# Performance work log

Hardware: AMD Instinct MI355X
Metric: run time of the kernel (lower is better)

The kernel has to match this reference:

```python
import jax, jax.numpy as jnp
import numpy as np

BATCH, IN, OUT, G = 2048, 512, 512, 8


def setup_inputs() -> dict:
    key = jax.random.key(0)
    k1, k2, k3 = jax.random.split(key, 3)
    x = jax.random.normal(k1, (BATCH, IN), dtype=jnp.float32)
    # spline coefficients, initialized small like normal_(c, 0, 0.001)
    c = jax.random.normal(k2, (G, OUT, IN), dtype=jnp.float32) * 0.001
    # residual weights, xavier-like small init
    w_b = jax.random.normal(k3, (OUT, IN), dtype=jnp.float32) * 0.001
    w_s = jnp.ones((OUT, IN), dtype=jnp.float32)
    # RBF grid centers over [-2, 2] (get_size() == G)
    grid = jnp.arange(G, dtype=jnp.float32) * (4.0 / (G - 1)) - 2.0
    return {"x": x, "c": c, "w_b": w_b, "w_s": w_s, "grid": grid}


def _basis(x, grid):
    # Gaussian RBF basis: [batch, G, in]
    d = x[:, None, :] - grid[None, :, None]
    return jnp.exp(-(d * d))


def reference(x, c, w_b, w_s, grid):
    basis_vals = _basis(x, grid)                      # [b, n=G, i]
    # faithful to th.einsum('bni,aoi->boi', ...): n and a are independently summed
    spline_out = jnp.einsum('bni,aoi->boi', basis_vals, c)  # [b, o, i]
    spline_out = spline_out * w_s[None]
    res_out = jax.nn.silu(x)[:, None, :] * w_b[None]  # [b, o, i]
    return (spline_out + res_out).sum(axis=-1)        # [b, o]
```

## Files before the change

### kernel.cpp

```cpp
#include <hip/hip_runtime.h>

#define BATCH 2048
#define IN    512
#define OUT   512
#define NG    8
#define KTOT  1024

#define BM 64
#define BN 64
#define BK 64
#define PAD 88
#define NIT (KTOT / BK)

typedef __attribute__((ext_vector_type(8))) short bf16x8;
typedef __attribute__((ext_vector_type(4))) float f32x4;

__device__ inline unsigned short f2bf(float f) {
    union { float f; unsigned int u; } v; v.f = f;
    unsigned int r = v.u + 0x7fffu + ((v.u >> 16) & 1u);
    return (unsigned short)(r >> 16);
}

__global__ __launch_bounds__(256) void prep_kernel(const float* __restrict__ x,
                                                   const float* __restrict__ c,
                                                   const float* __restrict__ w_b,
                                                   const float* __restrict__ w_s,
                                                   const float* __restrict__ grid,
                                                   unsigned short* __restrict__ A,
                                                   unsigned short* __restrict__ B) {
    int blk = blockIdx.x;
    int tid = threadIdx.x;
    if (blk < 512) {
        int e = (blk * 256 + tid) * 8;
        float g0 = grid[0];
        float dl = grid[1] - g0;
        float d2 = dl * dl;
        float dn[NG];
#pragma unroll
        for (int n = 0; n < NG; ++n) dn[n] = __expf(-d2 * (float)(n * n));
        float4 x0 = *(const float4*)&x[e];
        float4 x1 = *(const float4*)&x[e + 4];
        float xv[8] = {x0.x, x0.y, x0.z, x0.w, x1.x, x1.y, x1.z, x1.w};
        unsigned short sv[8], lv[8];
#pragma unroll
        for (int j = 0; j < 8; ++j) {
            float u  = xv[j] - g0;
            float e1 = __expf(-u * u);
            float q  = __expf(2.f * dl * u);
            float p  = dn[NG - 1];
#pragma unroll
            for (int n = NG - 2; n >= 0; --n) p = p * q + dn[n];
            sv[j] = f2bf(e1 * p);
            lv[j] = f2bf(xv[j] / (1.f + __expf(-xv[j])));
        }
        int b = e >> 9, i = e & 511;
        *(int4*)&A[b * KTOT + i]       = *(int4*)sv;
        *(int4*)&A[b * KTOT + 512 + i] = *(int4*)lv;
    } else {
        int e = ((blk - 512) * 256 + tid) * 8;
        float acc[8] = {};
#pragma unroll
        for (int a = 0; a < NG; ++a) {
            float4 c0 = *(const float4*)&c[(size_t)a * (OUT * IN) + e];
            float4 c1 = *(const float4*)&c[(size_t)a * (OUT * IN) + e + 4];
            acc[0] += c0.x; acc[1] += c0.y; acc[2] += c0.z; acc[3] += c0.w;
            acc[4] += c1.x; acc[5] += c1.y; acc[6] += c1.z; acc[7] += c1.w;
        }
        float4 s0 = *(const float4*)&w_s[e];
        float4 s1 = *(const float4*)&w_s[e + 4];
        float sw[8] = {s0.x, s0.y, s0.z, s0.w, s1.x, s1.y, s1.z, s1.w};
        float4 b0 = *(const float4*)&w_b[e];
        float4 b1 = *(const float4*)&w_b[e + 4];
        float bw[8] = {b0.x, b0.y, b0.z, b0.w, b1.x, b1.y, b1.z, b1.w};
        unsigned short cv[8], bv[8];
#pragma unroll
        for (int j = 0; j < 8; ++j) { cv[j] = f2bf(acc[j] * sw[j]); bv[j] = f2bf(bw[j]); }
        int o = e >> 9, i = e & 511;
        *(int4*)&B[o * KTOT + i]       = *(int4*)cv;
        *(int4*)&B[o * KTOT + 512 + i] = *(int4*)bv;
    }
}

__global__ __launch_bounds__(512) void gemm_kernel(const unsigned short* __restrict__ A,
                                                   const unsigned short* __restrict__ B,
                                                   float* __restrict__ outp) {
    __shared__ short As[2][BM * PAD];
    __shared__ short Bs[2][BN * PAD];

    int tid  = threadIdx.x;
    int lane = tid & 63;
    int w    = tid >> 6;
    int wm   = w >> 1, wn = w & 1;
    int lr   = lane & 15, lg = lane >> 4;

    int bid  = blockIdx.x;
    int mg   = bid & 7;
    int rest = bid >> 3;
    int sub  = rest >> 3;
    int ncol = rest & 7;
    int m0   = (mg * 4 + sub) * BM;
    int n0   = ncol * BN;

    int srow = tid >> 3;
    int sc8  = tid & 7;

    const int4* Ag = (const int4*)&A[(size_t)(m0 + srow) * KTOT + sc8 * 8];
    const int4* Bg = (const int4*)&B[(size_t)(n0 + srow) * KTOT + sc8 * 8];

    int wo = srow * PAD + sc8 * 8;

    f32x4 acc0 = {0.f, 0.f, 0.f, 0.f};
    f32x4 acc1 = {0.f, 0.f, 0.f, 0.f};

    int4 ca = Ag[0], cb = Bg[0];
    *(int4*)&As[0][wo] = ca;
    *(int4*)&Bs[0][wo] = cb;
    ca = Ag[8]; cb = Bg[8];
    __syncthreads();

#pragma unroll
    for (int it = 0; it < NIT; ++it) {
        int cur = it & 1;
        if (it + 1 < NIT) {
            *(int4*)&As[cur ^ 1][wo] = ca;
            *(int4*)&Bs[cur ^ 1][wo] = cb;
            if (it + 2 < NIT) { ca = Ag[(it + 2) * 8]; cb = Bg[(it + 2) * 8]; }
        }
#pragma unroll
        for (int ks = 0; ks < 2; ++ks) {
            bf16x8 a  = *(const bf16x8*)&As[cur][(wm * 16 + lr)      * PAD + ks * 32 + lg * 8];
            bf16x8 b0 = *(const bf16x8*)&Bs[cur][(wn * 32 + lr)      * PAD + ks * 32 + lg * 8];
            bf16x8 b1 = *(const bf16x8*)&Bs[cur][(wn * 32 + 16 + lr) * PAD + ks * 32 + lg * 8];
            acc0 = __builtin_amdgcn_mfma_f32_16x16x32_bf16(a, b0, acc0, 0, 0, 0);
            acc1 = __builtin_amdgcn_mfma_f32_16x16x32_bf16(a, b1, acc1, 0, 0, 0);
        }
        __syncthreads();
    }

    int orow = m0 + wm * 16 + lg * 4;
    int ocol = n0 + wn * 32 + lr;
#pragma unroll
    for (int r = 0; r < 4; ++r) {
        outp[(size_t)(orow + r) * OUT + ocol]      = acc0[r];
        outp[(size_t)(orow + r) * OUT + ocol + 16] = acc1[r];
    }
}

extern "C" void kernel_launch(void* const* d_in, const int* in_sizes, int n_in,
                              void* d_out, int out_size, void* d_ws, size_t ws_size,
                              hipStream_t stream) {
    (void)in_sizes; (void)n_in; (void)out_size; (void)ws_size;
    const float* x    = (const float*)d_in[0];
    const float* c    = (const float*)d_in[1];
    const float* w_b  = (const float*)d_in[2];
    const float* w_s  = (const float*)d_in[3];
    const float* grid = (const float*)d_in[4];
    float* outp = (float*)d_out;

    unsigned short* A = (unsigned short*)d_ws;
    unsigned short* B = A + (size_t)BATCH * KTOT;

    prep_kernel<<<512 + 128, 256, 0, stream>>>(x, c, w_b, w_s, grid, A, B);
    gemm_kernel<<<(BATCH / BM) * (OUT / BN), 512, 0, stream>>>(A, B, outp);
}
```

Measured before the change: 17.73 us.

## Fuse prep and GEMM into one kernel with a grid-wide atomic barrier

Merges the prep kernel and the GEMM kernel into a single launch of 256 blocks. Each block first builds its share of the bf16 A and B operands, then all blocks wait on an agent-scope atomic counter before starting the MFMA GEMM. This removes the second kernel launch and the gap between kernels, at the cost of a memset launch, a spin-wait barrier, and the assumption that all 256 blocks are resident at the same time.

```diff
diff --git a/kernel.cpp b/kernel.cpp
--- a/kernel.cpp
+++ b/kernel.cpp
@@ -11,6 +11,7 @@
 #define BK 64
 #define PAD 88
 #define NIT (KTOT / BK)
+#define NBLK 256
 
 typedef __attribute__((ext_vector_type(8))) short bf16x8;
 typedef __attribute__((ext_vector_type(4))) float f32x4;
@@ -21,23 +22,37 @@
     return (unsigned short)(r >> 16);
 }
 
-__global__ __launch_bounds__(256) void prep_kernel(const float* __restrict__ x,
-                                                   const float* __restrict__ c,
-                                                   const float* __restrict__ w_b,
-                                                   const float* __restrict__ w_s,
-                                                   const float* __restrict__ grid,
-                                                   unsigned short* __restrict__ A,
-                                                   unsigned short* __restrict__ B) {
-    int blk = blockIdx.x;
-    int tid = threadIdx.x;
-    if (blk < 512) {
-        int e = (blk * 256 + tid) * 8;
+__global__ __launch_bounds__(512) void fused_kernel(const float* __restrict__ x,
+                                                    const float* __restrict__ c,
+                                                    const float* __restrict__ w_b,
+                                                    const float* __restrict__ w_s,
+                                                    const float* __restrict__ grid,
+                                                    unsigned short* __restrict__ A,
+                                                    unsigned short* __restrict__ B,
+                                                    float* __restrict__ outp,
+                                                    unsigned int* __restrict__ flag) {
+    __shared__ short As[2][BM * PAD];
+    __shared__ short Bs[2][BN * PAD];
+
+    int tid  = threadIdx.x;
+    int bid  = blockIdx.x;
+    int mg   = bid & 7;
+    int rest = bid >> 3;
+    int sub  = rest >> 3;
+    int ncol = rest & 7;
+    int m0   = (mg * 4 + sub) * BM;
+    int n0   = ncol * BN;
+
+    {
+        int row = m0 + ncol * 8 + (tid >> 6);
+        int col = (tid & 63) * 8;
         float g0 = grid[0];
         float dl = grid[1] - g0;
         float d2 = dl * dl;
         float dn[NG];
 #pragma unroll
         for (int n = 0; n < NG; ++n) dn[n] = __expf(-d2 * (float)(n * n));
+        int e = row * IN + col;
         float4 x0 = *(const float4*)&x[e];
         float4 x1 = *(const float4*)&x[e + 4];
         float xv[8] = {x0.x, x0.y, x0.z, x0.w, x1.x, x1.y, x1.z, x1.w};
@@ -53,11 +68,14 @@
             sv[j] = f2bf(e1 * p);
             lv[j] = f2bf(xv[j] / (1.f + __expf(-xv[j])));
         }
-        int b = e >> 9, i = e & 511;
-        *(int4*)&A[b * KTOT + i]       = *(int4*)sv;
-        *(int4*)&A[b * KTOT + 512 + i] = *(int4*)lv;
-    } else {
-        int e = ((blk - 512) * 256 + tid) * 8;
+        *(int4*)&A[row * KTOT + col]       = *(int4*)sv;
+        *(int4*)&A[row * KTOT + 512 + col] = *(int4*)lv;
+    }
+
+    if (tid < 128) {
+        int row = bid * 2 + (tid >> 6);
+        int col = (tid & 63) * 8;
+        int e = row * IN + col;
         float acc[8] = {};
 #pragma unroll
         for (int a = 0; a < NG; ++a) {
@@ -75,38 +93,28 @@
         unsigned short cv[8], bv[8];
 #pragma unroll
         for (int j = 0; j < 8; ++j) { cv[j] = f2bf(acc[j] * sw[j]); bv[j] = f2bf(bw[j]); }
-        int o = e >> 9, i = e & 511;
-        *(int4*)&B[o * KTOT + i]       = *(int4*)cv;
-        *(int4*)&B[o * KTOT + 512 + i] = *(int4*)bv;
+        *(int4*)&B[row * KTOT + col]       = *(int4*)cv;
+        *(int4*)&B[row * KTOT + 512 + col] = *(int4*)bv;
     }
-}
 
-__global__ __launch_bounds__(512) void gemm_kernel(const unsigned short* __restrict__ A,
-                                                   const unsigned short* __restrict__ B,
-                                                   float* __restrict__ outp) {
-    __shared__ short As[2][BM * PAD];
-    __shared__ short Bs[2][BN * PAD];
+    __syncthreads();
+    if (tid == 0)
+        __hip_atomic_fetch_add(flag, 1u, __ATOMIC_ACQ_REL, __HIP_MEMORY_SCOPE_AGENT);
+    while (__hip_atomic_load(flag, __ATOMIC_RELAXED, __HIP_MEMORY_SCOPE_AGENT) < NBLK)
+        __builtin_amdgcn_s_sleep(8);
+    (void)__hip_atomic_load(flag, __ATOMIC_ACQUIRE, __HIP_MEMORY_SCOPE_AGENT);
+    __syncthreads();
 
-    int tid  = threadIdx.x;
     int lane = tid & 63;
     int w    = tid >> 6;
     int wm   = w >> 1, wn = w & 1;
     int lr   = lane & 15, lg = lane >> 4;
-
-    int bid  = blockIdx.x;
-    int mg   = bid & 7;
-    int rest = bid >> 3;
-    int sub  = rest >> 3;
-    int ncol = rest & 7;
-    int m0   = (mg * 4 + sub) * BM;
-    int n0   = ncol * BN;
 
     int srow = tid >> 3;
     int sc8  = tid & 7;
 
     const int4* Ag = (const int4*)&A[(size_t)(m0 + srow) * KTOT + sc8 * 8];
     const int4* Bg = (const int4*)&B[(size_t)(n0 + srow) * KTOT + sc8 * 8];
-
     int wo = srow * PAD + sc8 * 8;
 
     f32x4 acc0 = {0.f, 0.f, 0.f, 0.f};
@@ -159,7 +167,8 @@
 
     unsigned short* A = (unsigned short*)d_ws;
     unsigned short* B = A + (size_t)BATCH * KTOT;
+    unsigned int* flag = (unsigned int*)((char*)d_ws + (8u << 20));
 
-    prep_kernel<<<512 + 128, 256, 0, stream>>>(x, c, w_b, w_s, grid, A, B);
-    gemm_kernel<<<(BATCH / BM) * (OUT / BN), 512, 0, stream>>>(A, B, outp);
+    hipMemsetAsync(flag, 0, sizeof(unsigned int), stream);
+    fused_kernel<<<NBLK, 512, 0, stream>>>(x, c, w_b, w_s, grid, A, B, outp, flag);
 }
```

Result: slower. 63.82 us (+259.9%).

## Split GEMM K across two blocks and within-block warps, reduce with atomics

Applied to the files above, without the earlier changes.

The GEMM kernel now splits the K dimension in half across two blocks, which doubles the grid to 512 blocks and halves the serial k-loop length. Inside each block the warps are re-partitioned so that warp pairs split the two k-substeps, and each warp computes a 32x32 tile with four MFMAs. Partial sums from the two k-substeps are reduced through shared memory. The two block halves are combined with float atomic adds into an output that is zeroed first with a memset. This targets the short serial loop and low occupancy of the original 256-block launch, at the cost of an extra memset, atomic traffic and a non-deterministic summation order.

```diff
diff --git a/kernel.cpp b/kernel.cpp
--- a/kernel.cpp
+++ b/kernel.cpp
@@ -10,7 +10,7 @@
 #define BN 64
 #define BK 64
 #define PAD 88
-#define NIT (KTOT / BK)
+#define NITH 8
 
 typedef __attribute__((ext_vector_type(8))) short bf16x8;
 typedef __attribute__((ext_vector_type(4))) float f32x4;
@@ -90,12 +90,16 @@
     int tid  = threadIdx.x;
     int lane = tid & 63;
     int w    = tid >> 6;
-    int wm   = w >> 1, wn = w & 1;
+    int wm   = (w >> 2) & 1;
+    int wn   = (w >> 1) & 1;
+    int ks   = w & 1;
     int lr   = lane & 15, lg = lane >> 4;
 
-    int bid  = blockIdx.x;
-    int mg   = bid & 7;
-    int rest = bid >> 3;
+    int bid   = blockIdx.x;
+    int tile  = bid & 255;
+    int khalf = bid >> 8;
+    int mg   = tile & 7;
+    int rest = tile >> 3;
     int sub  = rest >> 3;
     int ncol = rest & 7;
     int m0   = (mg * 4 + sub) * BM;
@@ -104,13 +108,14 @@
     int srow = tid >> 3;
     int sc8  = tid & 7;
 
-    const int4* Ag = (const int4*)&A[(size_t)(m0 + srow) * KTOT + sc8 * 8];
-    const int4* Bg = (const int4*)&B[(size_t)(n0 + srow) * KTOT + sc8 * 8];
-
+    const int4* Ag = (const int4*)&A[(size_t)(m0 + srow) * KTOT + khalf * (NITH * BK) + sc8 * 8];
+    const int4* Bg = (const int4*)&B[(size_t)(n0 + srow) * KTOT + khalf * (NITH * BK) + sc8 * 8];
     int wo = srow * PAD + sc8 * 8;
 
-    f32x4 acc0 = {0.f, 0.f, 0.f, 0.f};
-    f32x4 acc1 = {0.f, 0.f, 0.f, 0.f};
+    f32x4 acc00 = {0.f, 0.f, 0.f, 0.f};
+    f32x4 acc01 = {0.f, 0.f, 0.f, 0.f};
+    f32x4 acc10 = {0.f, 0.f, 0.f, 0.f};
+    f32x4 acc11 = {0.f, 0.f, 0.f, 0.f};
 
     int4 ca = Ag[0], cb = Bg[0];
     *(int4*)&As[0][wo] = ca;
@@ -119,30 +124,47 @@
     __syncthreads();
 
 #pragma unroll
-    for (int it = 0; it < NIT; ++it) {
+    for (int it = 0; it < NITH; ++it) {
         int cur = it & 1;
-        if (it + 1 < NIT) {
+        if (it + 1 < NITH) {
             *(int4*)&As[cur ^ 1][wo] = ca;
             *(int4*)&Bs[cur ^ 1][wo] = cb;
-            if (it + 2 < NIT) { ca = Ag[(it + 2) * 8]; cb = Bg[(it + 2) * 8]; }
+            if (it + 2 < NITH) { ca = Ag[(it + 2) * 8]; cb = Bg[(it + 2) * 8]; }
         }
-#pragma unroll
-        for (int ks = 0; ks < 2; ++ks) {
-            bf16x8 a  = *(const bf16x8*)&As[cur][(wm * 16 + lr)      * PAD + ks * 32 + lg * 8];
-            bf16x8 b0 = *(const bf16x8*)&Bs[cur][(wn * 32 + lr)      * PAD + ks * 32 + lg * 8];
-            bf16x8 b1 = *(const bf16x8*)&Bs[cur][(wn * 32 + 16 + lr) * PAD + ks * 32 + lg * 8];
-            acc0 = __builtin_amdgcn_mfma_f32_16x16x32_bf16(a, b0, acc0, 0, 0, 0);
-            acc1 = __builtin_amdgcn_mfma_f32_16x16x32_bf16(a, b1, acc1, 0, 0, 0);
-        }
+        bf16x8 a0 = *(const bf16x8*)&As[cur][(wm * 32 + lr)      * PAD + ks * 32 + lg * 8];
+        bf16x8 a1 = *(const bf16x8*)&As[cur][(wm * 32 + 16 + lr) * PAD + ks * 32 + lg * 8];
+        bf16x8 b0 = *(const bf16x8*)&Bs[cur][(wn * 32 + lr)      * PAD + ks * 32 + lg * 8];
+        bf16x8 b1 = *(const bf16x8*)&Bs[cur][(wn * 32 + 16 + lr) * PAD + ks * 32 + lg * 8];
+        acc00 = __builtin_amdgcn_mfma_f32_16x16x32_bf16(a0, b0, acc00, 0, 0, 0);
+        acc01 = __builtin_amdgcn_mfma_f32_16x16x32_bf16(a0, b1, acc01, 0, 0, 0);
+        acc10 = __builtin_amdgcn_mfma_f32_16x16x32_bf16(a1, b0, acc10, 0, 0, 0);
+        acc11 = __builtin_amdgcn_mfma_f32_16x16x32_bf16(a1, b1, acc11, 0, 0, 0);
         __syncthreads();
     }
 
-    int orow = m0 + wm * 16 + lg * 4;
-    int ocol = n0 + wn * 32 + lr;
+    float* Ls = (float*)&As[0][0];
+    int p = w >> 1;
+    if (ks == 1) {
+        *(f32x4*)&Ls[p * 1024 + lane * 16 + 0]  = acc00;
+        *(f32x4*)&Ls[p * 1024 + lane * 16 + 4]  = acc01;
+        *(f32x4*)&Ls[p * 1024 + lane * 16 + 8]  = acc10;
+        *(f32x4*)&Ls[p * 1024 + lane * 16 + 12] = acc11;
+    }
+    __syncthreads();
+    if (ks == 0) {
+        f32x4 p00 = *(const f32x4*)&Ls[p * 1024 + lane * 16 + 0];
+        f32x4 p01 = *(const f32x4*)&Ls[p * 1024 + lane * 16 + 4];
+        f32x4 p10 = *(const f32x4*)&Ls[p * 1024 + lane * 16 + 8];
+        f32x4 p11 = *(const f32x4*)&Ls[p * 1024 + lane * 16 + 12];
+        int orow = m0 + wm * 32 + lg * 4;
+        int ocol = n0 + wn * 32 + lr;
 #pragma unroll
-    for (int r = 0; r < 4; ++r) {
-        outp[(size_t)(orow + r) * OUT + ocol]      = acc0[r];
-        outp[(size_t)(orow + r) * OUT + ocol + 16] = acc1[r];
+        for (int r = 0; r < 4; ++r) {
+            unsafeAtomicAdd(&outp[(size_t)(orow + r) * OUT + ocol],           acc00[r] + p00[r]);
+            unsafeAtomicAdd(&outp[(size_t)(orow + r) * OUT + ocol + 16],      acc01[r] + p01[r]);
+            unsafeAtomicAdd(&outp[(size_t)(orow + 16 + r) * OUT + ocol],      acc10[r] + p10[r]);
+            unsafeAtomicAdd(&outp[(size_t)(orow + 16 + r) * OUT + ocol + 16], acc11[r] + p11[r]);
+        }
     }
 }
 
@@ -160,6 +182,7 @@
     unsigned short* A = (unsigned short*)d_ws;
     unsigned short* B = A + (size_t)BATCH * KTOT;
 
+    hipMemsetAsync(d_out, 0, (size_t)BATCH * OUT * sizeof(float), stream);
     prep_kernel<<<512 + 128, 256, 0, stream>>>(x, c, w_b, w_s, grid, A, B);
-    gemm_kernel<<<(BATCH / BM) * (OUT / BN), 512, 0, stream>>>(A, B, outp);
+    gemm_kernel<<<512, 512, 0, stream>>>(A, B, outp);
 }
```

Measured after the change: 26.97 us. +52.1%, slower.
